# Performance work log

Hardware: AMD Instinct MI355X
Metric: run time of the kernel (lower is better)

The kernel has to match this reference:

```python
import jax, jax.numpy as jnp
import numpy as np

L = 8          # number of GNN layers / graph variants
B = 128        # graphs per batch
NL = 32        # ligand nodes per graph
NP = 256       # protein nodes per graph
N_LIG = B * NL     # 4096
N_PROT = B * NP    # 32768
E_PL_G = 1024      # protein->ligand edges per graph
E_LL_G = 256       # ligand->ligand edges per graph
E_PL = B * E_PL_G  # 131072
E_LL = B * E_LL_G  # 32768
F_IN = 128
H = 256
OUT = 2


def _block_edges(key, n_per_graph, e_per_graph):
    # random node indices, offset so edges stay within each graph of the batch
    idx = jax.random.randint(key, (L, B, e_per_graph), 0, n_per_graph)
    off = (jnp.arange(B) * n_per_graph)[None, :, None]
    return (idx + off).reshape(L, B * e_per_graph).astype(jnp.int32)


def setup_inputs() -> dict:
    key = jax.random.key(0)
    ks = jax.random.split(key, 12)
    feat_lig = jax.random.normal(ks[0], (L, N_LIG, F_IN), jnp.float32)
    feat_prot = jax.random.normal(ks[1], (L, N_PROT, F_IN), jnp.float32)
    src_pl = _block_edges(ks[2], NP, E_PL_G)   # protein src indices
    dst_pl = _block_edges(ks[3], NL, E_PL_G)   # ligand dst indices
    src_ll = _block_edges(ks[4], NL, E_LL_G)
    dst_ll = _block_edges(ks[5], NL, E_LL_G)
    s = 1.0 / np.sqrt(F_IN)
    W_pl = jax.random.normal(ks[6], (L, F_IN, H), jnp.float32) * s
    b_pl = jnp.zeros((L, H), jnp.float32)
    W_ll = jax.random.normal(ks[7], (L, F_IN, H), jnp.float32) * s
    b_ll = jnp.zeros((L, H), jnp.float32)
    W_fc = jax.random.normal(ks[8], (L * H, OUT), jnp.float32) / np.sqrt(L * H)
    b_fc = jnp.zeros((OUT,), jnp.float32)
    return dict(feat_lig=feat_lig, feat_prot=feat_prot,
                src_pl=src_pl, dst_pl=dst_pl, src_ll=src_ll, dst_ll=dst_ll,
                W_pl=W_pl, b_pl=b_pl, W_ll=W_ll, b_ll=b_ll,
                W_fc=W_fc, b_fc=b_fc)


def _gconv(x_src, W, b, src, dst, n_src, n_dst):
    # DGL GraphConv with norm='both': D_dst^-1/2 * A^T * D_src^-1/2 * X W + b
    ones = jnp.ones(src.shape[0], x_src.dtype)
    deg_src = jnp.clip(jax.ops.segment_sum(ones, src, num_segments=n_src), 1.0)
    deg_dst = jnp.clip(jax.ops.segment_sum(ones, dst, num_segments=n_dst), 1.0)
    xw = (x_src * jax.lax.rsqrt(deg_src)[:, None]) @ W          # [n_src,H]
    agg = jax.ops.segment_sum(xw[src], dst, num_segments=n_dst)  # [n_dst,H]
    return agg * jax.lax.rsqrt(deg_dst)[:, None] + b


def reference(feat_lig, feat_prot, src_pl, dst_pl, src_ll, dst_ll,
              W_pl, b_pl, W_ll, b_ll, W_fc, b_fc):
    def layer(fl, fp, Wp, bp, Wl, bl, spl, dpl, sll, dll):
        # HeteroGraphConv sum-aggregates the two relations with dst='ligand'
        h = (_gconv(fp, Wp, bp, spl, dpl, N_PROT, N_LIG)
             + _gconv(fl, Wl, bl, sll, dll, N_LIG, N_LIG))      # [N_LIG,H]
        # unbatch + per-graph mean over ligand nodes (equal-size graphs)
        return h.reshape(B, NL, H).mean(axis=1)                  # [B,H]

    h8 = jax.vmap(layer)(feat_lig, feat_prot, W_pl, b_pl, W_ll, b_ll,
                         src_pl, dst_pl, src_ll, dst_ll)         # [L,B,H]
    combined = jnp.transpose(h8, (1, 0, 2)).reshape(B, L * H)    # cat dim=1
    return jax.nn.sigmoid(combined @ W_fc + b_fc)                # [B,OUT]
```

## Files before the change

### kernel.cpp

```cpp
#include <hip/hip_runtime.h>

#define L 8
#define B 128
#define NL 32
#define NP 256
#define EPL_G 1024
#define ELL_G 256
#define FIN 128
#define H 256
#define OUT 2

typedef float f4 __attribute__((ext_vector_type(4)));

__shared__ int s_cnt_src[NP];
__shared__ int s_cnt_dst[NL];
__shared__ float s_c[NP];
__shared__ f4 s_red[16][32];

template <int REL>
__device__ __forceinline__ void agg_block(
    int l, int b, int tid,
    const float* __restrict__ feat,
    const int* __restrict__ srcA, const int* __restrict__ dstA,
    float* __restrict__ gout)
{
    constexpr int E  = REL ? ELL_G : EPL_G;
    constexpr int NS = REL ? NL : NP;

    const int* srcp = srcA + (size_t)l * (B * E) + (size_t)b * E;
    const int* dstp = dstA + (size_t)l * (B * E) + (size_t)b * E;

    for (int i = tid; i < NS; i += 512) { s_cnt_src[i] = 0; s_c[i] = 0.f; }
    if (tid < NL) s_cnt_dst[tid] = 0;
    __syncthreads();

    int es[2], ed[2];
    int ne = 0;
#pragma unroll
    for (int e = tid; e < E; e += 512) {
        int s = srcp[e] - b * NS;
        int d = dstp[e] - b * NL;
        es[ne] = s; ed[ne] = d; ne++;
        atomicAdd(&s_cnt_src[s], 1);
        atomicAdd(&s_cnt_dst[d], 1);
    }
    __syncthreads();
#pragma unroll
    for (int i = 0; i < (E + 511) / 512; i++)
        if (i < ne) atomicAdd(&s_c[es[i]], rsqrtf((float)s_cnt_dst[ed[i]]));
    __syncthreads();
    for (int i = tid; i < NS; i += 512) {
        int c = s_cnt_src[i];
        s_c[i] = c ? s_c[i] * rsqrtf((float)c) * (1.0f / NL) : 0.f;
    }
    __syncthreads();

    const int lane = tid & 63;
    const int wave = tid >> 6;
    const int slot = wave * 2 + (lane >> 5);
    const int col  = lane & 31;
    const float* fb = feat + ((size_t)(l * B + b)) * NS * FIN + col * 4;

    f4 acc0 = 0.f, acc1 = 0.f;
#pragma unroll
    for (int r0 = 0; r0 < NS; r0 += 32) {
        int ra = r0 + slot;
        int rb = ra + 16;
        float wa = s_c[ra];
        float wb = s_c[rb];
        f4 va = __builtin_nontemporal_load((const f4*)(fb + (size_t)ra * FIN));
        f4 vb = __builtin_nontemporal_load((const f4*)(fb + (size_t)rb * FIN));
        acc0 += wa * va;
        acc1 += wb * vb;
    }
    s_red[slot][col] = acc0 + acc1;
    __syncthreads();

    if (tid < FIN) {
        float t = 0.f;
#pragma unroll
        for (int k = 0; k < 16; k++) {
            const float* p = (const float*)&s_red[k][tid >> 2];
            t += p[tid & 3];
        }
        gout[((size_t)(l * B + b)) * FIN + tid] = t;
    }
}

__global__ __launch_bounds__(512) void mega_kernel(
    const float* __restrict__ feat_lig, const float* __restrict__ feat_prot,
    const int* __restrict__ src_pl, const int* __restrict__ dst_pl,
    const int* __restrict__ src_ll, const int* __restrict__ dst_ll,
    const float* __restrict__ W_pl, const float* __restrict__ W_ll,
    const float* __restrict__ W_fc,
    const float* __restrict__ b_pl, const float* __restrict__ b_ll,
    const float* __restrict__ b_fc,
    float* __restrict__ g_pl, float* __restrict__ g_ll,
    float* __restrict__ Wc_pl, float* __restrict__ Wc_ll,
    float* __restrict__ bias_out)
{
    const int bid = blockIdx.x;
    const int tid = threadIdx.x;

    if (bid < L * B) {
        agg_block<0>(bid >> 7, bid & 127, tid, feat_prot, src_pl, dst_pl, g_pl);
    } else if (bid < 2 * L * B) {
        const int lb = bid - L * B;
        agg_block<1>(lb >> 7, lb & 127, tid, feat_lig, src_ll, dst_ll, g_ll);
    } else if (bid < 2 * L * B + 16) {
        const int q = bid - 2 * L * B;
        const int l = q & 7;
        const float* W = (q >> 3) ? W_ll : W_pl;
        float* outc    = (q >> 3) ? Wc_ll : Wc_pl;
        if (tid < 256) {
            const int f = tid >> 1, o = tid & 1;
            const float* wrow = W + ((size_t)l * FIN + f) * H;
            const float* fc   = W_fc + (size_t)l * H * OUT + o;
            float acc = 0.f;
#pragma unroll 4
            for (int h = 0; h < H; h++)
                acc += wrow[h] * fc[h * OUT];
            outc[((size_t)l * FIN + f) * OUT + o] = acc;
        }
    } else {
        float* r0 = (float*)s_red;
        float* r1 = r0 + 512;
        float a0 = 0.f, a1 = 0.f;
        for (int i = tid; i < L * H; i += 512) {
            float bs = b_pl[i] + b_ll[i];
            a0 += bs * W_fc[i * OUT];
            a1 += bs * W_fc[i * OUT + 1];
        }
        r0[tid] = a0; r1[tid] = a1;
        __syncthreads();
        for (int s = 256; s > 0; s >>= 1) {
            if (tid < s) { r0[tid] += r0[tid + s]; r1[tid] += r1[tid + s]; }
            __syncthreads();
        }
        if (tid == 0) {
            bias_out[0] = r0[0] + b_fc[0];
            bias_out[1] = r1[0] + b_fc[1];
        }
    }
}

__global__ __launch_bounds__(256) void final_kernel(
    const float* __restrict__ g_pl, const float* __restrict__ g_ll,
    const float* __restrict__ Wc_pl, const float* __restrict__ Wc_ll,
    const float* __restrict__ bias_out, float* __restrict__ out)
{
    const int b = blockIdx.x;
    const int t = threadIdx.x;
    const int o = t >> 7, f = t & 127;
    float acc = 0.f;
#pragma unroll
    for (int l = 0; l < L; l++) {
        float gp = g_pl[((size_t)(l * B + b)) * FIN + f];
        float gl = g_ll[((size_t)(l * B + b)) * FIN + f];
        acc += gp * Wc_pl[((size_t)l * FIN + f) * OUT + o]
             + gl * Wc_ll[((size_t)l * FIN + f) * OUT + o];
    }
    __shared__ float red[256];
    red[t] = acc;
    __syncthreads();
    for (int s = 64; s > 0; s >>= 1) {
        if (f < s) red[t] += red[t + s];
        __syncthreads();
    }
    if (f == 0) {
        float x = red[o << 7] + bias_out[o];
        out[b * OUT + o] = 1.0f / (1.0f + expf(-x));
    }
}

extern "C" void kernel_launch(void* const* d_in, const int* in_sizes, int n_in,
                              void* d_out, int out_size, void* d_ws, size_t ws_size,
                              hipStream_t stream) {
    const float* feat_lig  = (const float*)d_in[0];
    const float* feat_prot = (const float*)d_in[1];
    const int* src_pl = (const int*)d_in[2];
    const int* dst_pl = (const int*)d_in[3];
    const int* src_ll = (const int*)d_in[4];
    const int* dst_ll = (const int*)d_in[5];
    const float* W_pl = (const float*)d_in[6];
    const float* b_pl = (const float*)d_in[7];
    const float* W_ll = (const float*)d_in[8];
    const float* b_ll = (const float*)d_in[9];
    const float* W_fc = (const float*)d_in[10];
    const float* b_fc = (const float*)d_in[11];
    float* out = (float*)d_out;

    float* ws       = (float*)d_ws;
    float* g_pl     = ws;
    float* g_ll     = g_pl + (size_t)L * B * FIN;
    float* Wc_pl    = g_ll + (size_t)L * B * FIN;
    float* Wc_ll    = Wc_pl + (size_t)L * FIN * OUT;
    float* bias_out = Wc_ll + (size_t)L * FIN * OUT;

    mega_kernel<<<dim3(2 * L * B + 17), 512, 0, stream>>>(
        feat_lig, feat_prot, src_pl, dst_pl, src_ll, dst_ll,
        W_pl, W_ll, W_fc, b_pl, b_ll, b_fc,
        g_pl, g_ll, Wc_pl, Wc_ll, bias_out);
    final_kernel<<<dim3(B), 256, 0, stream>>>(g_pl, g_ll, Wc_pl, Wc_ll, bias_out, out);
}
```

Measured before the change: 225.2 us.

## Split degree-weight prep from feature aggregation and fold FC projection into agg

Moves the per-graph edge-degree coefficient computation into a separate prep kernel that writes the coefficients to workspace. A new agg kernel then handles both relations per (layer, graph) block, streams the features, and applies the precomputed W·W_fc projection in place to produce per-layer partial logits. This replaces the 128-block final reduction with a single-block sum. In exchange it adds a kernel launch and a workspace round trip for the coefficients, and it serializes the edge-counting phase ahead of the feature streaming rather than running them in the same blocks.

```diff
diff --git a/kernel.cpp b/kernel.cpp
--- a/kernel.cpp
+++ b/kernel.cpp
@@ -12,165 +12,188 @@
 
 typedef float f4 __attribute__((ext_vector_type(4)));
 
-__shared__ int s_cnt_src[NP];
-__shared__ int s_cnt_dst[NL];
-__shared__ float s_c[NP];
-__shared__ f4 s_red[16][32];
-
 template <int REL>
-__device__ __forceinline__ void agg_block(
+__device__ __forceinline__ void calc_c(
     int l, int b, int tid,
-    const float* __restrict__ feat,
     const int* __restrict__ srcA, const int* __restrict__ dstA,
-    float* __restrict__ gout)
+    float* __restrict__ cout,
+    int* cnt_src, int* cnt_dst, float* cacc)
 {
     constexpr int E  = REL ? ELL_G : EPL_G;
     constexpr int NS = REL ? NL : NP;
-
     const int* srcp = srcA + (size_t)l * (B * E) + (size_t)b * E;
     const int* dstp = dstA + (size_t)l * (B * E) + (size_t)b * E;
 
-    for (int i = tid; i < NS; i += 512) { s_cnt_src[i] = 0; s_c[i] = 0.f; }
-    if (tid < NL) s_cnt_dst[tid] = 0;
-    __syncthreads();
-
-    int es[2], ed[2];
-    int ne = 0;
-#pragma unroll
-    for (int e = tid; e < E; e += 512) {
-        int s = srcp[e] - b * NS;
-        int d = dstp[e] - b * NL;
-        es[ne] = s; ed[ne] = d; ne++;
-        atomicAdd(&s_cnt_src[s], 1);
-        atomicAdd(&s_cnt_dst[d], 1);
-    }
-    __syncthreads();
-#pragma unroll
-    for (int i = 0; i < (E + 511) / 512; i++)
-        if (i < ne) atomicAdd(&s_c[es[i]], rsqrtf((float)s_cnt_dst[ed[i]]));
-    __syncthreads();
-    for (int i = tid; i < NS; i += 512) {
-        int c = s_cnt_src[i];
-        s_c[i] = c ? s_c[i] * rsqrtf((float)c) * (1.0f / NL) : 0.f;
-    }
-    __syncthreads();
-
-    const int lane = tid & 63;
-    const int wave = tid >> 6;
-    const int slot = wave * 2 + (lane >> 5);
-    const int col  = lane & 31;
-    const float* fb = feat + ((size_t)(l * B + b)) * NS * FIN + col * 4;
-
-    f4 acc0 = 0.f, acc1 = 0.f;
-#pragma unroll
-    for (int r0 = 0; r0 < NS; r0 += 32) {
-        int ra = r0 + slot;
-        int rb = ra + 16;
-        float wa = s_c[ra];
-        float wb = s_c[rb];
-        f4 va = __builtin_nontemporal_load((const f4*)(fb + (size_t)ra * FIN));
-        f4 vb = __builtin_nontemporal_load((const f4*)(fb + (size_t)rb * FIN));
-        acc0 += wa * va;
-        acc1 += wb * vb;
-    }
-    s_red[slot][col] = acc0 + acc1;
-    __syncthreads();
-
-    if (tid < FIN) {
-        float t = 0.f;
-#pragma unroll
-        for (int k = 0; k < 16; k++) {
-            const float* p = (const float*)&s_red[k][tid >> 2];
-            t += p[tid & 3];
-        }
-        gout[((size_t)(l * B + b)) * FIN + tid] = t;
-    }
-}
-
-__global__ __launch_bounds__(512) void mega_kernel(
-    const float* __restrict__ feat_lig, const float* __restrict__ feat_prot,
+    __syncthreads();
+    for (int i = tid; i < NS; i += 256) { cnt_src[i] = 0; cacc[i] = 0.f; }
+    if (tid < NL) cnt_dst[tid] = 0;
+    __syncthreads();
+
+    int es[E / 256], ed[E / 256];
+#pragma unroll
+    for (int k = 0; k < E / 256; k++) {
+        int e = tid + k * 256;
+        es[k] = srcp[e] - b * NS;
+        ed[k] = dstp[e] - b * NL;
+        atomicAdd(&cnt_src[es[k]], 1);
+        atomicAdd(&cnt_dst[ed[k]], 1);
+    }
+    __syncthreads();
+#pragma unroll
+    for (int k = 0; k < E / 256; k++)
+        atomicAdd(&cacc[es[k]], rsqrtf((float)cnt_dst[ed[k]]));
+    __syncthreads();
+    for (int i = tid; i < NS; i += 256) {
+        int c = cnt_src[i];
+        cout[((size_t)(l * B + b)) * NS + i] =
+            c ? cacc[i] * rsqrtf((float)c) * (1.0f / NL) : 0.f;
+    }
+}
+
+__global__ __launch_bounds__(256) void prep_kernel(
     const int* __restrict__ src_pl, const int* __restrict__ dst_pl,
     const int* __restrict__ src_ll, const int* __restrict__ dst_ll,
     const float* __restrict__ W_pl, const float* __restrict__ W_ll,
     const float* __restrict__ W_fc,
     const float* __restrict__ b_pl, const float* __restrict__ b_ll,
     const float* __restrict__ b_fc,
-    float* __restrict__ g_pl, float* __restrict__ g_ll,
+    float* __restrict__ c_pl, float* __restrict__ c_ll,
     float* __restrict__ Wc_pl, float* __restrict__ Wc_ll,
     float* __restrict__ bias_out)
 {
-    const int bid = blockIdx.x;
-    const int tid = threadIdx.x;
+    const int bid = blockIdx.x, tid = threadIdx.x;
+    __shared__ int    cnt_src[NP];
+    __shared__ int    cnt_dst[NL];
+    __shared__ float  cacc[NP];
+    __shared__ float2 sfc[H];
+    __shared__ float  br[2][256];
 
     if (bid < L * B) {
-        agg_block<0>(bid >> 7, bid & 127, tid, feat_prot, src_pl, dst_pl, g_pl);
-    } else if (bid < 2 * L * B) {
-        const int lb = bid - L * B;
-        agg_block<1>(lb >> 7, lb & 127, tid, feat_lig, src_ll, dst_ll, g_ll);
-    } else if (bid < 2 * L * B + 16) {
-        const int q = bid - 2 * L * B;
+        const int l = bid >> 7, b = bid & 127;
+        calc_c<0>(l, b, tid, src_pl, dst_pl, c_pl, cnt_src, cnt_dst, cacc);
+        calc_c<1>(l, b, tid, src_ll, dst_ll, c_ll, cnt_src, cnt_dst, cacc);
+    } else if (bid < L * B + 16) {
+        const int q = bid - L * B;
         const int l = q & 7;
         const float* W = (q >> 3) ? W_ll : W_pl;
         float* outc    = (q >> 3) ? Wc_ll : Wc_pl;
-        if (tid < 256) {
-            const int f = tid >> 1, o = tid & 1;
-            const float* wrow = W + ((size_t)l * FIN + f) * H;
-            const float* fc   = W_fc + (size_t)l * H * OUT + o;
-            float acc = 0.f;
+        sfc[tid] = ((const float2*)W_fc)[(size_t)l * H + tid];
+        __syncthreads();
+        if (tid < FIN) {
+            const float* wrow = W + ((size_t)l * FIN + tid) * H;
+            float a0 = 0.f, a1 = 0.f;
 #pragma unroll 4
-            for (int h = 0; h < H; h++)
-                acc += wrow[h] * fc[h * OUT];
-            outc[((size_t)l * FIN + f) * OUT + o] = acc;
+            for (int h = 0; h < H; h += 4) {
+                f4 w = *(const f4*)(wrow + h);
+                float2 c0 = sfc[h], c1 = sfc[h + 1], c2 = sfc[h + 2], c3 = sfc[h + 3];
+                a0 += w.x * c0.x + w.y * c1.x + w.z * c2.x + w.w * c3.x;
+                a1 += w.x * c0.y + w.y * c1.y + w.z * c2.y + w.w * c3.y;
+            }
+            ((float2*)outc)[(size_t)l * FIN + tid] = make_float2(a0, a1);
         }
     } else {
-        float* r0 = (float*)s_red;
-        float* r1 = r0 + 512;
         float a0 = 0.f, a1 = 0.f;
-        for (int i = tid; i < L * H; i += 512) {
+        for (int i = tid; i < L * H; i += 256) {
             float bs = b_pl[i] + b_ll[i];
-            a0 += bs * W_fc[i * OUT];
-            a1 += bs * W_fc[i * OUT + 1];
-        }
-        r0[tid] = a0; r1[tid] = a1;
+            float2 w = ((const float2*)W_fc)[i];
+            a0 += bs * w.x;
+            a1 += bs * w.y;
+        }
+        br[0][tid] = a0; br[1][tid] = a1;
         __syncthreads();
-        for (int s = 256; s > 0; s >>= 1) {
-            if (tid < s) { r0[tid] += r0[tid + s]; r1[tid] += r1[tid + s]; }
+        for (int s = 128; s > 0; s >>= 1) {
+            if (tid < s) { br[0][tid] += br[0][tid + s]; br[1][tid] += br[1][tid + s]; }
             __syncthreads();
         }
         if (tid == 0) {
-            bias_out[0] = r0[0] + b_fc[0];
-            bias_out[1] = r1[0] + b_fc[1];
-        }
+            bias_out[0] = br[0][0] + b_fc[0];
+            bias_out[1] = br[1][0] + b_fc[1];
+        }
+    }
+}
+
+__global__ __launch_bounds__(512) void agg_kernel(
+    const float* __restrict__ feat_lig, const float* __restrict__ feat_prot,
+    const float* __restrict__ c_pl, const float* __restrict__ c_ll,
+    const float* __restrict__ Wc_pl, const float* __restrict__ Wc_ll,
+    float* __restrict__ partial)
+{
+    __shared__ float sc_p[NP];
+    __shared__ float sc_l[NL];
+    __shared__ f4    sred[2][16][32];
+    __shared__ float spart[2][4];
+
+    const int bid = blockIdx.x;
+    const int l = bid >> 7, b = bid & 127;
+    const int tid = threadIdx.x;
+
+    if (tid < NP)            sc_p[tid]      = c_pl[((size_t)(l * B + b)) * NP + tid];
+    else if (tid < NP + NL)  sc_l[tid - NP] = c_ll[((size_t)(l * B + b)) * NL + (tid - NP)];
+    __syncthreads();
+
+    const int lane = tid & 63;
+    const int wave = tid >> 6;
+    const int slot = wave * 2 + (lane >> 5);
+    const int col  = lane & 31;
+
+    const float* fp = feat_prot + ((size_t)(l * B + b)) * NP * FIN + col * 4;
+    const float* fl = feat_lig  + ((size_t)(l * B + b)) * NL * FIN + col * 4;
+
+    f4 vl0 = __builtin_nontemporal_load((const f4*)(fl + (size_t)slot * FIN));
+    f4 vl1 = __builtin_nontemporal_load((const f4*)(fl + (size_t)(slot + 16) * FIN));
+
+    f4 acc0 = 0.f, acc1 = 0.f;
+#pragma unroll
+    for (int r0 = 0; r0 < NP; r0 += 32) {
+        int ra = r0 + slot;
+        int rb = ra + 16;
+        f4 va = __builtin_nontemporal_load((const f4*)(fp + (size_t)ra * FIN));
+        f4 vb = __builtin_nontemporal_load((const f4*)(fp + (size_t)rb * FIN));
+        acc0 += sc_p[ra] * va;
+        acc1 += sc_p[rb] * vb;
+    }
+    sred[0][slot][col] = acc0 + acc1;
+    sred[1][slot][col] = sc_l[slot] * vl0 + sc_l[slot + 16] * vl1;
+    __syncthreads();
+
+    float pr0 = 0.f, pr1 = 0.f;
+    if (tid < 256) {
+        const int rel = tid >> 7, f = tid & 127;
+        float g = 0.f;
+#pragma unroll
+        for (int k = 0; k < 16; k++) {
+            const float* p = (const float*)&sred[rel][k][f >> 2];
+            g += p[f & 3];
+        }
+        const float* Wc = rel ? Wc_ll : Wc_pl;
+        float2 w = ((const float2*)Wc)[(size_t)l * FIN + f];
+        pr0 = g * w.x;
+        pr1 = g * w.y;
+    }
+#pragma unroll
+    for (int off = 32; off > 0; off >>= 1) {
+        pr0 += __shfl_down(pr0, off);
+        pr1 += __shfl_down(pr1, off);
+    }
+    if (lane == 0 && wave < 4) { spart[0][wave] = pr0; spart[1][wave] = pr1; }
+    __syncthreads();
+    if (tid == 0) {
+        float s0 = spart[0][0] + spart[0][1] + spart[0][2] + spart[0][3];
+        float s1 = spart[1][0] + spart[1][1] + spart[1][2] + spart[1][3];
+        ((float2*)partial)[(size_t)l * B + b] = make_float2(s0, s1);
     }
 }
 
 __global__ __launch_bounds__(256) void final_kernel(
-    const float* __restrict__ g_pl, const float* __restrict__ g_ll,
-    const float* __restrict__ Wc_pl, const float* __restrict__ Wc_ll,
-    const float* __restrict__ bias_out, float* __restrict__ out)
-{
-    const int b = blockIdx.x;
+    const float* __restrict__ partial, const float* __restrict__ bias_out,
+    float* __restrict__ out)
+{
     const int t = threadIdx.x;
-    const int o = t >> 7, f = t & 127;
-    float acc = 0.f;
-#pragma unroll
-    for (int l = 0; l < L; l++) {
-        float gp = g_pl[((size_t)(l * B + b)) * FIN + f];
-        float gl = g_ll[((size_t)(l * B + b)) * FIN + f];
-        acc += gp * Wc_pl[((size_t)l * FIN + f) * OUT + o]
-             + gl * Wc_ll[((size_t)l * FIN + f) * OUT + o];
-    }
-    __shared__ float red[256];
-    red[t] = acc;
-    __syncthreads();
-    for (int s = 64; s > 0; s >>= 1) {
-        if (f < s) red[t] += red[t + s];
-        __syncthreads();
-    }
-    if (f == 0) {
-        float x = red[o << 7] + bias_out[o];
-        out[b * OUT + o] = 1.0f / (1.0f + expf(-x));
-    }
+    float acc = bias_out[t & 1];
+#pragma unroll
+    for (int l = 0; l < L; l++)
+        acc += partial[(size_t)l * (B * OUT) + t];
+    out[t] = 1.0f / (1.0f + expf(-acc));
 }
 
 extern "C" void kernel_launch(void* const* d_in, const int* in_sizes, int n_in,
@@ -191,15 +214,17 @@
     float* out = (float*)d_out;
 
     float* ws       = (float*)d_ws;
-    float* g_pl     = ws;
-    float* g_ll     = g_pl + (size_t)L * B * FIN;
-    float* Wc_pl    = g_ll + (size_t)L * B * FIN;
+    float* c_pl     = ws;
+    float* c_ll     = c_pl  + (size_t)L * B * NP;
+    float* Wc_pl    = c_ll  + (size_t)L * B * NL;
     float* Wc_ll    = Wc_pl + (size_t)L * FIN * OUT;
     float* bias_out = Wc_ll + (size_t)L * FIN * OUT;
-
-    mega_kernel<<<dim3(2 * L * B + 17), 512, 0, stream>>>(
-        feat_lig, feat_prot, src_pl, dst_pl, src_ll, dst_ll,
-        W_pl, W_ll, W_fc, b_pl, b_ll, b_fc,
-        g_pl, g_ll, Wc_pl, Wc_ll, bias_out);
-    final_kernel<<<dim3(B), 256, 0, stream>>>(g_pl, g_ll, Wc_pl, Wc_ll, bias_out, out);
-}
+    float* partial  = bias_out + 2;
+
+    prep_kernel<<<dim3(L * B + 17), 256, 0, stream>>>(
+        src_pl, dst_pl, src_ll, dst_ll, W_pl, W_ll, W_fc, b_pl, b_ll, b_fc,
+        c_pl, c_ll, Wc_pl, Wc_ll, bias_out);
+    agg_kernel<<<dim3(L * B), 512, 0, stream>>>(
+        feat_lig, feat_prot, c_pl, c_ll, Wc_pl, Wc_ll, partial);
+    final_kernel<<<dim3(1), 256, 0, stream>>>(partial, bias_out, out);
+}
```

New measurement: 225.7 us. No clear change (+0.2%).
